# Performance work log

Hardware: AMD Instinct MI355X
Metric: run time of the kernel (lower is better)

## Reference

```python
import jax, jax.numpy as jnp
import numpy as np

A, B, S, E, H = 8, 64, 128, 512, 512


def _xavier(key, shape):
    fan_in, fan_out = shape[-2], shape[-1]
    limit = float(np.sqrt(6.0 / (fan_in + fan_out)))
    return jax.random.uniform(key, shape, jnp.float32, -limit, limit)


def setup_inputs() -> dict:
    key = jax.random.key(0)
    ks = jax.random.split(key, 8)
    inp = {
        "x": jax.random.normal(ks[0], (A, B, S, E), jnp.float32),
        "input2r": _xavier(ks[1], (A, E, H)),
        "input2z": _xavier(ks[2], (A, E, H)),
        "input2n": _xavier(ks[3], (A, E, H)),
        "hidden2r": _xavier(ks[4], (A, H, H)),
        "hidden2z": _xavier(ks[5], (A, H, H)),
        "hidden2n": _xavier(ks[6], (A, H, H)),
        "input2r_bias": jnp.zeros((A, H), jnp.float32),
        "input2z_bias": jnp.zeros((A, H), jnp.float32),
        "input2n_bias": jnp.zeros((A, H), jnp.float32),
        "hidden2r_bias": jnp.zeros((A, H), jnp.float32),
        "hidden2z_bias": jnp.zeros((A, H), jnp.float32),
        "hidden2n_bias": jnp.zeros((A, H), jnp.float32),
    }
    return inp


def _gru(x, input2r, input2z, input2n, input2r_bias, input2z_bias, input2n_bias,
         hidden2r, hidden2z, hidden2n, hidden2r_bias, hidden2z_bias, hidden2n_bias):
    # Precompute the input projections for all timesteps at once (same math,
    # hoisted out of the sequential loop): [A,B,S,H] -> scan over S.
    xr = jnp.einsum('abse,aeh->absh', x, input2r) + input2r_bias[:, None, None, :]
    xz = jnp.einsum('abse,aeh->absh', x, input2z) + input2z_bias[:, None, None, :]
    xn = jnp.einsum('abse,aeh->absh', x, input2n) + input2n_bias[:, None, None, :]
    # scan carries h: [A,B,H]; inputs have leading S axis.
    xr_t = jnp.moveaxis(xr, 2, 0)  # [S,A,B,H]
    xz_t = jnp.moveaxis(xz, 2, 0)
    xn_t = jnp.moveaxis(xn, 2, 0)

    hrb = hidden2r_bias[:, None, :]
    hzb = hidden2z_bias[:, None, :]
    hnb = hidden2n_bias[:, None, :]

    def step(h, inputs):
        xr_i, xz_i, xn_i = inputs
        r = jax.nn.sigmoid(xr_i + jnp.einsum('abh,ahk->abk', h, hidden2r) + hrb)
        z = jax.nn.sigmoid(xz_i + jnp.einsum('abh,ahk->abk', h, hidden2z) + hzb)
        n = jnp.tanh(xn_i + r * (jnp.einsum('abh,ahk->abk', h, hidden2n) + hnb))
        h_new = (1.0 - z) * n + z * h
        return h_new, h_new

    h0 = jnp.zeros((x.shape[0], x.shape[1], hidden2r.shape[-1]), x.dtype)
    h_last, outs = jax.lax.scan(step, h0, (xr_t, xz_t, xn_t))
    outputs = jnp.moveaxis(outs, 0, 2)  # [A,B,S,H]
    return outputs, h_last


def reference(x, input2r, input2z, input2n, input2r_bias, input2z_bias, input2n_bias,
              hidden2r, hidden2z, hidden2n, hidden2r_bias, hidden2z_bias, hidden2n_bias):
    return _gru(x, input2r, input2z, input2n, input2r_bias, input2z_bias, input2n_bias,
                hidden2r, hidden2z, hidden2n, hidden2r_bias, hidden2z_bias, hidden2n_bias)
```

## Files before the change

kernel.cpp:

```cpp
#include <hip/hip_runtime.h>

#define A_ 8
#define B_ 64
#define S_ 128
#define E_ 512
#define H_ 512

typedef float f32x4 __attribute__((ext_vector_type(4)));
typedef short s16x8 __attribute__((ext_vector_type(8)));

__device__ __forceinline__ float sigm(float v)   { return 1.f / (1.f + __expf(-v)); }
__device__ __forceinline__ float tanh_f(float v) { return 2.f / (1.f + __expf(-2.f * v)) - 1.f; }

__device__ __forceinline__ unsigned short f2bf(float f) {
  unsigned u = __builtin_bit_cast(unsigned, f);
  u += 0x7fffu + ((u >> 16) & 1u);
  return (unsigned short)(u >> 16);
}
__device__ __forceinline__ float bf2f(unsigned short b) {
  return __builtin_bit_cast(float, ((unsigned)b) << 16);
}

union U2 { unsigned long long u[2]; s16x8 v; };
union PK { uint4 u; unsigned short h[8]; };
union PH { s16x8 v; unsigned short h[8]; };

__global__ __launch_bounds__(256, 2) void gru_proj(
    const float* __restrict__ x,
    const float* __restrict__ wri, const float* __restrict__ wzi, const float* __restrict__ wni,
    const float* __restrict__ bri, const float* __restrict__ bzi, const float* __restrict__ bni,
    const float* __restrict__ brh, const float* __restrict__ bzh,
    unsigned* __restrict__ xprz, float* __restrict__ xn_arr)
{
  const int n0   = blockIdx.x * 64;
  const int b    = blockIdx.y;
  const int a    = blockIdx.z;
  const int tid  = threadIdx.x;
  const int lane = tid & 63;
  const int wid  = tid >> 6;
  const int l15  = lane & 15;
  const int l4   = lane >> 4;

  const float* xp = x + (size_t)(a * B_ + b) * S_ * E_;

  __shared__ short Af[4096];
  __shared__ short Bf[6144];

  f32x4 acc[3][2][4];
#pragma unroll
  for (int g = 0; g < 3; ++g)
#pragma unroll
    for (int m = 0; m < 2; ++m)
#pragma unroll
      for (int c = 0; c < 4; ++c) acc[g][m][c] = (f32x4){0.f, 0.f, 0.f, 0.f};

  const int am = tid >> 1;
  const int ah = tid & 1;

  for (int kt = 0; kt < E_; kt += 32) {
    const float* ap = xp + (size_t)am * E_ + kt + ah * 16;
    float4 a0 = *(const float4*)(ap);
    float4 a1 = *(const float4*)(ap + 4);
    float4 a2 = *(const float4*)(ap + 8);
    float4 a3 = *(const float4*)(ap + 12);
    PH pa0, pa1;
    pa0.h[0]=f2bf(a0.x); pa0.h[1]=f2bf(a0.y); pa0.h[2]=f2bf(a0.z); pa0.h[3]=f2bf(a0.w);
    pa0.h[4]=f2bf(a1.x); pa0.h[5]=f2bf(a1.y); pa0.h[6]=f2bf(a1.z); pa0.h[7]=f2bf(a1.w);
    pa1.h[0]=f2bf(a2.x); pa1.h[1]=f2bf(a2.y); pa1.h[2]=f2bf(a2.z); pa1.h[3]=f2bf(a2.w);
    pa1.h[4]=f2bf(a3.x); pa1.h[5]=f2bf(a3.y); pa1.h[6]=f2bf(a3.z); pa1.h[7]=f2bf(a3.w);
    int au = (am >> 4) * 64 + (ah * 2) * 16 + (am & 15);
    ((s16x8*)Af)[au]      = pa0.v;
    ((s16x8*)Af)[au + 16] = pa1.v;

#pragma unroll
    for (int ii = 0; ii < 3; ++ii) {
      int idx  = tid + ii * 256;
      int gate = idx >> 8;
      int rem  = idx & 255;
      int l    = rem & 63;
      int col  = n0 + ((rem >> 6) << 4) + (l & 15);
      int kb   = kt + (l >> 4) * 8;
      const float* W = gate == 0 ? wri : gate == 1 ? wzi : wni;
      const float* wp2 = W + (size_t)(a * E_ + kb) * H_ + col;
      PH pb;
#pragma unroll
      for (int j = 0; j < 8; ++j) pb.h[j] = f2bf(wp2[(size_t)j * H_]);
      ((s16x8*)Bf)[idx] = pb.v;
    }
    __syncthreads();

    s16x8 av0 = ((s16x8*)Af)[(wid * 2 + 0) * 64 + lane];
    s16x8 av1 = ((s16x8*)Af)[(wid * 2 + 1) * 64 + lane];
#pragma unroll
    for (int g = 0; g < 3; ++g)
#pragma unroll
      for (int cs = 0; cs < 4; ++cs) {
        s16x8 bv = ((s16x8*)Bf)[g * 256 + cs * 64 + lane];
        acc[g][0][cs] = __builtin_amdgcn_mfma_f32_16x16x32_bf16(av0, bv, acc[g][0][cs], 0, 0, 0);
        acc[g][1][cs] = __builtin_amdgcn_mfma_f32_16x16x32_bf16(av1, bv, acc[g][1][cs], 0, 0, 0);
      }
    __syncthreads();
  }

#pragma unroll
  for (int cs = 0; cs < 4; ++cs) {
    int col = n0 + cs * 16 + l15;
    float br = bri[a * H_ + col] + brh[a * H_ + col];
    float bz = bzi[a * H_ + col] + bzh[a * H_ + col];
    float bn = bni[a * H_ + col];
#pragma unroll
    for (int m = 0; m < 2; ++m) {
#pragma unroll
      for (int i = 0; i < 4; ++i) {
        int srow = wid * 32 + m * 16 + l4 * 4 + i;
        size_t base = ((size_t)(a * S_ + srow) * B_ + b) * H_ + col;
        float rv = acc[0][m][cs][i] + br;
        float zv = acc[1][m][cs][i] + bz;
        float nv = acc[2][m][cs][i] + bn;
        xprz[base]   = (unsigned)f2bf(rv) | ((unsigned)f2bf(zv) << 16);
        xn_arr[base] = nv;
      }
    }
  }
}

__global__ __launch_bounds__(256, 1) void gru_scan(
    const unsigned* __restrict__ xprz, const float* __restrict__ xn_arr,
    const float* __restrict__ wrh, const float* __restrict__ wzh, const float* __restrict__ wnh,
    const float* __restrict__ bnh,
    float* __restrict__ out, float* __restrict__ hlast,
    unsigned short* __restrict__ hbuf0, unsigned short* __restrict__ hbuf1,
    int* __restrict__ flags)
{
  __shared__ uint4 wflat[6144];

  const int wg    = blockIdx.x;
  const int G     = wg & 15;
  const int a     = G >> 1;
  const int hf    = G & 1;
  const int slice = wg >> 4;
  const int tid   = threadIdx.x;
  const int lane  = tid & 63;
  const int w     = tid >> 6;
  const int l15   = lane & 15;
  const int l4    = lane >> 4;
  const int mt    = w & 1;
  const int nt    = w >> 1;

  for (int idx = tid; idx < 6144; idx += 256) {
    int gate = idx >> 11;
    int rem  = idx & 2047;
    int kk   = rem >> 7;
    int rem2 = rem & 127;
    int nt_  = rem2 >> 6;
    int l    = rem2 & 63;
    int col   = slice * 32 + nt_ * 16 + (l & 15);
    int kbase = kk * 32 + (l >> 4) * 8;
    const float* W = gate == 0 ? wrh : gate == 1 ? wzh : wnh;
    const float* wp = W + ((size_t)(a * H_ + kbase)) * H_ + col;
    PK pk;
#pragma unroll
    for (int j = 0; j < 8; ++j) pk.h[j] = f2bf(wp[(size_t)j * H_]);
    wflat[idx] = pk.u;
  }
  __syncthreads();

  const int nc    = slice * 32 + nt * 16 + l15;
  const float vbnh = bnh[a * H_ + nc];
  const int halfb = (a * 2 + hf) * 16384;
  const int hbase = halfb + l4 * 256 + (mt * 16 + l15) * 8;
  int* flagsG = flags + G * (16 * 32);

  float hold[4] = {0.f, 0.f, 0.f, 0.f};
  float xr_[4], xz_[4], xn_[4];

#pragma unroll
  for (int i = 0; i < 4; ++i) {
    int b = hf * 32 + mt * 16 + l4 * 4 + i;
    size_t xo = ((size_t)(a * S_ + 0) * B_ + b) * H_ + nc;
    unsigned prz = xprz[xo];
    xr_[i] = bf2f((unsigned short)(prz & 0xffff));
    xz_[i] = bf2f((unsigned short)(prz >> 16));
    xn_[i] = xn_arr[xo];
  }

  const f32x4 zero4 = {0.f, 0.f, 0.f, 0.f};

  for (int s = 0; s < S_; ++s) {
    const unsigned short* hprev = (s & 1) ? hbuf0 : hbuf1;
    unsigned short*       hcur  = (s & 1) ? hbuf1 : hbuf0;

    U2 hh[16];
#pragma unroll
    for (int kk = 0; kk < 16; ++kk) {
      unsigned long long* p = (unsigned long long*)(hprev + hbase + kk * 1024);
      hh[kk].u[0] = __hip_atomic_load(p,     __ATOMIC_RELAXED, __HIP_MEMORY_SCOPE_AGENT);
      hh[kk].u[1] = __hip_atomic_load(p + 1, __ATOMIC_RELAXED, __HIP_MEMORY_SCOPE_AGENT);
    }
    f32x4 aR = zero4, aZ = zero4, aHN = zero4;
#pragma unroll
    for (int kk = 0; kk < 16; ++kk) {
      s16x8 bR = __builtin_bit_cast(s16x8, wflat[kk * 128        + nt * 64 + lane]);
      s16x8 bZ = __builtin_bit_cast(s16x8, wflat[2048 + kk * 128 + nt * 64 + lane]);
      s16x8 bN = __builtin_bit_cast(s16x8, wflat[4096 + kk * 128 + nt * 64 + lane]);
      aR  = __builtin_amdgcn_mfma_f32_16x16x32_bf16(hh[kk].v, bR, aR, 0, 0, 0);
      aZ  = __builtin_amdgcn_mfma_f32_16x16x32_bf16(hh[kk].v, bZ, aZ, 0, 0, 0);
      aHN = __builtin_amdgcn_mfma_f32_16x16x32_bf16(hh[kk].v, bN, aHN, 0, 0, 0);
    }

    float hn4[4];
#pragma unroll
    for (int i = 0; i < 4; ++i) {
      float rg = sigm(xr_[i] + aR[i]);
      float zg = sigm(xz_[i] + aZ[i]);
      float ng = tanh_f(xn_[i] + rg * (aHN[i] + vbnh));
      hn4[i] = (1.f - zg) * ng + zg * hold[i];
      hold[i] = hn4[i];
    }

#pragma unroll
    for (int i = 0; i < 4; ++i) {
      int r = mt * 16 + l4 * 4 + i;
      unsigned short nb = f2bf(hn4[i]);
      unsigned other = __shfl_xor((unsigned)nb, 1);
      if ((lane & 1) == 0) {
        unsigned val = (unsigned)nb | (other << 16);
        __hip_atomic_store((unsigned*)(hcur + halfb + (nc >> 3) * 256 + r * 8 + (nc & 6)),
                           val, __ATOMIC_RELAXED, __HIP_MEMORY_SCOPE_AGENT);
      }
    }
    __syncthreads();
    asm volatile("" ::: "memory");
    if (tid == 0)
      __hip_atomic_store(flagsG + slice * 32, s + 1,
                         __ATOMIC_RELAXED, __HIP_MEMORY_SCOPE_AGENT);

#pragma unroll
    for (int i = 0; i < 4; ++i) {
      int b = hf * 32 + mt * 16 + l4 * 4 + i;
      out[((size_t)(a * B_ + b) * S_ + s) * H_ + nc] = hn4[i];
    }
    if (s == S_ - 1) {
#pragma unroll
      for (int i = 0; i < 4; ++i) {
        int b = hf * 32 + mt * 16 + l4 * 4 + i;
        hlast[(size_t)(a * B_ + b) * H_ + nc] = hn4[i];
      }
    } else {
#pragma unroll
      for (int i = 0; i < 4; ++i) {
        int b = hf * 32 + mt * 16 + l4 * 4 + i;
        size_t xo = ((size_t)(a * S_ + (s + 1)) * B_ + b) * H_ + nc;
        unsigned prz = xprz[xo];
        xr_[i] = bf2f((unsigned short)(prz & 0xffff));
        xz_[i] = bf2f((unsigned short)(prz >> 16));
        xn_[i] = xn_arr[xo];
      }
      const int target = s + 1;
      for (;;) {
        int v = __hip_atomic_load(flagsG + (lane & 15) * 32,
                                  __ATOMIC_RELAXED, __HIP_MEMORY_SCOPE_AGENT);
        if (__all(v >= target)) break;
      }
      asm volatile("" ::: "memory");
    }
  }
}

__global__ __launch_bounds__(256, 1) void gru_persist(
    const float* __restrict__ x,
    const float* __restrict__ wri, const float* __restrict__ wzi, const float* __restrict__ wni,
    const float* __restrict__ wrh, const float* __restrict__ wzh, const float* __restrict__ wnh,
    const float* __restrict__ bri, const float* __restrict__ bzi, const float* __restrict__ bni,
    const float* __restrict__ brh, const float* __restrict__ bzh, const float* __restrict__ bnh,
    float* __restrict__ out, float* __restrict__ hlast,
    unsigned short* __restrict__ hbuf0, unsigned short* __restrict__ hbuf1,
    int* __restrict__ flags)
{
  __shared__ uint4 wflat[6144];
  const int wg = blockIdx.x, a = wg >> 5, slice = wg & 31, n0 = slice << 4;
  const int tid = threadIdx.x, lane = tid & 63, wid = tid >> 6;
  const int l15 = lane & 15, l4 = lane >> 4, b0w = wid << 4;

  for (int idx = tid; idx < 6144; idx += 256) {
    int set = idx / 3072, rem = idx - set * 3072, gate = rem >> 10;
    int rem2 = rem & 1023, kk = rem2 >> 6, l = rem2 & 63;
    int c = l & 15, kbase = kk * 32 + (l >> 4) * 8;
    const float* W = (set == 0) ? (gate == 0 ? wri : gate == 1 ? wzi : wni)
                                : (gate == 0 ? wrh : gate == 1 ? wzh : wnh);
    const float* wp = W + ((size_t)(a * 512 + kbase)) * 512 + n0 + c;
    PK pk;
#pragma unroll
    for (int j = 0; j < 8; ++j) pk.h[j] = f2bf(wp[(size_t)j * 512]);
    wflat[idx] = pk.u;
  }
  __syncthreads();

  const int nc = n0 + l15;
  const float vbri = bri[a*512+nc], vbzi = bzi[a*512+nc], vbni = bni[a*512+nc];
  const float vbrh = brh[a*512+nc], vbzh = bzh[a*512+nc], vbnh = bnh[a*512+nc];
  const float* xrow = x + (size_t)(a * 64 + b0w + l15) * 65536 + l4 * 8;
  const int hbase = ((a * 64 + l4) * 64 + b0w + l15) * 8;
  int* flagsA = flags + a * 64;
  const f32x4 zero4 = {0.f, 0.f, 0.f, 0.f};
  f32x4 aR, aZ, aXN, aHN;

  auto xpart = [&](int sv) {
    const float* xp = xrow + (size_t)sv * 512;
    aR = zero4; aZ = zero4; aXN = zero4;
#pragma unroll
    for (int kk = 0; kk < 16; ++kk) {
      float4 x0 = *reinterpret_cast<const float4*>(xp + kk * 32);
      float4 x1 = *reinterpret_cast<const float4*>(xp + kk * 32 + 4);
      PH af;
      af.h[0]=f2bf(x0.x); af.h[1]=f2bf(x0.y); af.h[2]=f2bf(x0.z); af.h[3]=f2bf(x0.w);
      af.h[4]=f2bf(x1.x); af.h[5]=f2bf(x1.y); af.h[6]=f2bf(x1.z); af.h[7]=f2bf(x1.w);
      s16x8 bR = __builtin_bit_cast(s16x8, wflat[(kk)*64+lane]);
      s16x8 bZ = __builtin_bit_cast(s16x8, wflat[(16+kk)*64+lane]);
      s16x8 bN = __builtin_bit_cast(s16x8, wflat[(32+kk)*64+lane]);
      aR  = __builtin_amdgcn_mfma_f32_16x16x32_bf16(af.v, bR, aR, 0,0,0);
      aZ  = __builtin_amdgcn_mfma_f32_16x16x32_bf16(af.v, bZ, aZ, 0,0,0);
      aXN = __builtin_amdgcn_mfma_f32_16x16x32_bf16(af.v, bN, aXN, 0,0,0);
    }
  };

  xpart(0);
  for (int s = 0; s < S_; ++s) {
    const unsigned short* hprev = (s & 1) ? hbuf0 : hbuf1;
    unsigned short*       hcur  = (s & 1) ? hbuf1 : hbuf0;
    aHN = zero4;
#pragma unroll
    for (int kk = 0; kk < 16; ++kk) {
      unsigned long long* p = (unsigned long long*)(hprev + hbase + kk * 2048);
      U2 uu;
      uu.u[0] = __hip_atomic_load(p,   __ATOMIC_RELAXED, __HIP_MEMORY_SCOPE_AGENT);
      uu.u[1] = __hip_atomic_load(p+1, __ATOMIC_RELAXED, __HIP_MEMORY_SCOPE_AGENT);
      s16x8 bR = __builtin_bit_cast(s16x8, wflat[(48+kk)*64+lane]);
      s16x8 bZ = __builtin_bit_cast(s16x8, wflat[(64+kk)*64+lane]);
      s16x8 bN = __builtin_bit_cast(s16x8, wflat[(80+kk)*64+lane]);
      aR  = __builtin_amdgcn_mfma_f32_16x16x32_bf16(uu.v, bR, aR, 0,0,0);
      aZ  = __builtin_amdgcn_mfma_f32_16x16x32_bf16(uu.v, bZ, aZ, 0,0,0);
      aHN = __builtin_amdgcn_mfma_f32_16x16x32_bf16(uu.v, bN, aHN, 0,0,0);
    }
#pragma unroll
    for (int i = 0; i < 4; ++i) {
      int r = b0w + l4 * 4 + i;
      unsigned* hop = (unsigned*)(hprev + ((a*64 + (nc>>3))*64 + r)*8 + (nc&6));
      unsigned pair = __hip_atomic_load(hop, __ATOMIC_RELAXED, __HIP_MEMORY_SCOPE_AGENT);
      float hold = bf2f((nc & 1) ? (unsigned short)(pair >> 16) : (unsigned short)(pair & 0xffff));
      float rg = sigm(aR[i] + vbri + vbrh);
      float zg = sigm(aZ[i] + vbzi + vbzh);
      float ng = tanh_f(aXN[i] + vbni + rg * (aHN[i] + vbnh));
      float hnew = (1.f - zg) * ng + zg * hold;
      out[((size_t)(a*64 + r)*128 + s)*512 + nc] = hnew;
      if (s == S_ - 1) hlast[(size_t)(a*64 + r)*512 + nc] = hnew;
      unsigned short nb = f2bf(hnew);
      unsigned other = __shfl_xor((unsigned)nb, 1);
      if ((lane & 1) == 0) {
        unsigned val = (unsigned)nb | (other << 16);
        __hip_atomic_store((unsigned*)(hcur + ((a*64 + (nc>>3))*64 + r)*8 + (nc&6)),
                           val, __ATOMIC_RELAXED, __HIP_MEMORY_SCOPE_AGENT);
      }
    }
    __syncthreads();
    if (tid == 0)
      __hip_atomic_store(flagsA + slice, s + 1, __ATOMIC_RELEASE, __HIP_MEMORY_SCOPE_AGENT);
    if (s < S_ - 1) {
      xpart(s + 1);
      const int target = s + 1;
      for (;;) {
        int v = __hip_atomic_load(flagsA + (lane & 31), __ATOMIC_ACQUIRE, __HIP_MEMORY_SCOPE_AGENT);
        if (__all(v >= target)) break;
        __builtin_amdgcn_s_sleep(1);
      }
    }
  }
}

extern "C" void kernel_launch(void* const* d_in, const int* in_sizes, int n_in,
                              void* d_out, int out_size, void* d_ws, size_t ws_size,
                              hipStream_t stream)
{
  const float* x   = (const float*)d_in[0];
  const float* wri = (const float*)d_in[1];
  const float* wzi = (const float*)d_in[2];
  const float* wni = (const float*)d_in[3];
  const float* wrh = (const float*)d_in[4];
  const float* wzh = (const float*)d_in[5];
  const float* wnh = (const float*)d_in[6];
  const float* bri = (const float*)d_in[7];
  const float* bzi = (const float*)d_in[8];
  const float* bni = (const float*)d_in[9];
  const float* brh = (const float*)d_in[10];
  const float* bzh = (const float*)d_in[11];
  const float* bnh = (const float*)d_in[12];

  float* out   = (float*)d_out;
  float* hlast = out + (size_t)A_ * B_ * S_ * H_;

  const size_t XPRZ  = (size_t)A_ * S_ * B_ * H_;
  const size_t HBUF  = (size_t)A_ * 64 * 64 * 8;
  const size_t FLAGS_B = (size_t)16 * 16 * 32 * sizeof(int);
  const size_t need_new = XPRZ * 4 * 2 + HBUF * 2 * 2 + FLAGS_B;
  const size_t need_old = HBUF * 2 * 2 + 2048;

  if (ws_size >= need_new) {
    unsigned* xprz = (unsigned*)d_ws;
    float* xn_arr  = (float*)((char*)d_ws + XPRZ * 4);
    unsigned short* hbuf0 = (unsigned short*)((char*)d_ws + XPRZ * 8);
    unsigned short* hbuf1 = hbuf0 + HBUF;
    int* flags = (int*)(hbuf1 + HBUF);
    hipMemsetAsync(hbuf0, 0, HBUF * 2 * 2 + FLAGS_B, stream);
    gru_proj<<<dim3(8, 64, 8), 256, 0, stream>>>(x, wri, wzi, wni,
                                                 bri, bzi, bni, brh, bzh,
                                                 xprz, xn_arr);
    gru_scan<<<256, 256, 0, stream>>>(xprz, xn_arr, wrh, wzh, wnh, bnh,
                                      out, hlast, hbuf0, hbuf1, flags);
  } else if (ws_size >= need_old) {
    unsigned short* hbuf0 = (unsigned short*)d_ws;
    unsigned short* hbuf1 = hbuf0 + HBUF;
    int* flags = (int*)(hbuf1 + HBUF);
    hipMemsetAsync(d_ws, 0, need_old, stream);
    gru_persist<<<256, 256, 0, stream>>>(x, wri, wzi, wni, wrh, wzh, wnh,
                                         bri, bzi, bni, brh, bzh, bnh,
                                         out, hlast, hbuf0, hbuf1, flags);
  }
}
```

Before: 764.5 us.

## Pre-convert input weights to bf16 fragments and split scan flag wait into halves

Adds a small kernel that converts the input-projection weights to bf16 once, already laid out as MFMA fragments. The projection kernel then loads these with one vector read per fragment instead of strided fp32 loads and per-block conversion, which were repeated across all 64 batch blocks. In the scan kernel, the hidden state for the next step is now loaded right after the flag wait. The wait is split in two: the first 8 producer flags are checked and their half of h is loaded before waiting on the rest, so loads overlap the remaining synchronisation. This costs an extra launch and workspace for the fragment buffer.

```diff
diff --git a/kernel.cpp b/kernel.cpp
--- a/kernel.cpp
+++ b/kernel.cpp
@@ -25,14 +25,41 @@
 union PK { uint4 u; unsigned short h[8]; };
 union PH { s16x8 v; unsigned short h[8]; };
 
+__global__ __launch_bounds__(256) void gru_wconv(
+    const float* __restrict__ wri, const float* __restrict__ wzi,
+    const float* __restrict__ wni, s16x8* __restrict__ wfrag)
+{
+  const int bid = blockIdx.x;
+  const int kt  = bid & 15;
+  const int ag  = bid >> 4;
+  const int g   = ag % 3;
+  const int a   = ag / 3;
+  const float* W = g == 0 ? wri : g == 1 ? wzi : wni;
+  const int t  = threadIdx.x;
+  const int l  = t & 63;
+  const int cs = (t >> 6) & 3;
+  const int colbase = cs * 16 + (l & 15);
+  const int kb = kt * 32 + (l >> 4) * 8;
+  const float* wp0 = W + (size_t)(a * E_ + kb) * H_;
+#pragma unroll
+  for (int nt = 0; nt < 8; ++nt) {
+    const float* wp = wp0 + nt * 64 + colbase;
+    PH pb;
+#pragma unroll
+    for (int j = 0; j < 8; ++j) pb.h[j] = f2bf(wp[(size_t)j * H_]);
+    wfrag[((size_t)bid * 8 + nt) * 256 + t] = pb.v;
+  }
+}
+
 __global__ __launch_bounds__(256, 2) void gru_proj(
     const float* __restrict__ x,
-    const float* __restrict__ wri, const float* __restrict__ wzi, const float* __restrict__ wni,
+    const s16x8* __restrict__ wfrag,
     const float* __restrict__ bri, const float* __restrict__ bzi, const float* __restrict__ bni,
     const float* __restrict__ brh, const float* __restrict__ bzh,
     unsigned* __restrict__ xprz, float* __restrict__ xn_arr)
 {
-  const int n0   = blockIdx.x * 64;
+  const int ntI  = blockIdx.x;
+  const int n0   = ntI * 64;
   const int b    = blockIdx.y;
   const int a    = blockIdx.z;
   const int tid  = threadIdx.x;
@@ -42,6 +69,7 @@
   const int l4   = lane >> 4;
 
   const float* xp = x + (size_t)(a * B_ + b) * S_ * E_;
+  const s16x8* wfA = wfrag + ((size_t)a * 3) * 16 * 8 * 256;
 
   __shared__ short Af[4096];
   __shared__ short Bf[6144];
@@ -58,6 +86,7 @@
   const int ah = tid & 1;
 
   for (int kt = 0; kt < E_; kt += 32) {
+    const int kti = kt >> 5;
     const float* ap = xp + (size_t)am * E_ + kt + ah * 16;
     float4 a0 = *(const float4*)(ap);
     float4 a1 = *(const float4*)(ap + 4);
@@ -74,18 +103,10 @@
 
 #pragma unroll
     for (int ii = 0; ii < 3; ++ii) {
-      int idx  = tid + ii * 256;
-      int gate = idx >> 8;
-      int rem  = idx & 255;
-      int l    = rem & 63;
-      int col  = n0 + ((rem >> 6) << 4) + (l & 15);
-      int kb   = kt + (l >> 4) * 8;
-      const float* W = gate == 0 ? wri : gate == 1 ? wzi : wni;
-      const float* wp2 = W + (size_t)(a * E_ + kb) * H_ + col;
-      PH pb;
-#pragma unroll
-      for (int j = 0; j < 8; ++j) pb.h[j] = f2bf(wp2[(size_t)j * H_]);
-      ((s16x8*)Bf)[idx] = pb.v;
+      int idx = tid + ii * 256;
+      int g   = idx >> 8;
+      int rem = idx & 255;
+      ((s16x8*)Bf)[idx] = wfA[(((size_t)g * 16 + kti) * 8 + ntI) * 256 + rem];
     }
     __syncthreads();
 
@@ -186,17 +207,13 @@
 
   const f32x4 zero4 = {0.f, 0.f, 0.f, 0.f};
 
+  U2 hh[16];
+#pragma unroll
+  for (int kk = 0; kk < 16; ++kk) { hh[kk].u[0] = 0ull; hh[kk].u[1] = 0ull; }
+
   for (int s = 0; s < S_; ++s) {
-    const unsigned short* hprev = (s & 1) ? hbuf0 : hbuf1;
-    unsigned short*       hcur  = (s & 1) ? hbuf1 : hbuf0;
-
-    U2 hh[16];
-#pragma unroll
-    for (int kk = 0; kk < 16; ++kk) {
-      unsigned long long* p = (unsigned long long*)(hprev + hbase + kk * 1024);
-      hh[kk].u[0] = __hip_atomic_load(p,     __ATOMIC_RELAXED, __HIP_MEMORY_SCOPE_AGENT);
-      hh[kk].u[1] = __hip_atomic_load(p + 1, __ATOMIC_RELAXED, __HIP_MEMORY_SCOPE_AGENT);
-    }
+    unsigned short* hcur = (s & 1) ? hbuf1 : hbuf0;
+
     f32x4 aR = zero4, aZ = zero4, aHN = zero4;
 #pragma unroll
     for (int kk = 0; kk < 16; ++kk) {
@@ -258,11 +275,31 @@
       }
       const int target = s + 1;
       for (;;) {
-        int v = __hip_atomic_load(flagsG + (lane & 15) * 32,
+        int v = __hip_atomic_load(flagsG + (lane & 7) * 32,
                                   __ATOMIC_RELAXED, __HIP_MEMORY_SCOPE_AGENT);
         if (__all(v >= target)) break;
       }
       asm volatile("" ::: "memory");
+#pragma unroll
+      for (int kk = 0; kk < 8; ++kk) {
+        const unsigned long long* p =
+            (const unsigned long long*)(hcur + hbase + kk * 1024);
+        hh[kk].u[0] = __hip_atomic_load(p,     __ATOMIC_RELAXED, __HIP_MEMORY_SCOPE_AGENT);
+        hh[kk].u[1] = __hip_atomic_load(p + 1, __ATOMIC_RELAXED, __HIP_MEMORY_SCOPE_AGENT);
+      }
+      for (;;) {
+        int v = __hip_atomic_load(flagsG + ((lane & 7) + 8) * 32,
+                                  __ATOMIC_RELAXED, __HIP_MEMORY_SCOPE_AGENT);
+        if (__all(v >= target)) break;
+      }
+      asm volatile("" ::: "memory");
+#pragma unroll
+      for (int kk = 8; kk < 16; ++kk) {
+        const unsigned long long* p =
+            (const unsigned long long*)(hcur + hbase + kk * 1024);
+        hh[kk].u[0] = __hip_atomic_load(p,     __ATOMIC_RELAXED, __HIP_MEMORY_SCOPE_AGENT);
+        hh[kk].u[1] = __hip_atomic_load(p + 1, __ATOMIC_RELAXED, __HIP_MEMORY_SCOPE_AGENT);
+      }
     }
   }
 }
@@ -398,20 +435,23 @@
   float* out   = (float*)d_out;
   float* hlast = out + (size_t)A_ * B_ * S_ * H_;
 
-  const size_t XPRZ  = (size_t)A_ * S_ * B_ * H_;
-  const size_t HBUF  = (size_t)A_ * 64 * 64 * 8;
+  const size_t XPRZ    = (size_t)A_ * S_ * B_ * H_;
+  const size_t WFRAG   = (size_t)384 * 8 * 256;
+  const size_t HBUF    = (size_t)A_ * 64 * 64 * 8;
   const size_t FLAGS_B = (size_t)16 * 16 * 32 * sizeof(int);
-  const size_t need_new = XPRZ * 4 * 2 + HBUF * 2 * 2 + FLAGS_B;
-  const size_t need_old = HBUF * 2 * 2 + 2048;
+  const size_t need_new = XPRZ * 8 + WFRAG * 16 + HBUF * 4 + FLAGS_B;
+  const size_t need_old = HBUF * 4 + 2048;
 
   if (ws_size >= need_new) {
     unsigned* xprz = (unsigned*)d_ws;
     float* xn_arr  = (float*)((char*)d_ws + XPRZ * 4);
-    unsigned short* hbuf0 = (unsigned short*)((char*)d_ws + XPRZ * 8);
+    s16x8* wfrag   = (s16x8*)((char*)d_ws + XPRZ * 8);
+    unsigned short* hbuf0 = (unsigned short*)((char*)d_ws + XPRZ * 8 + WFRAG * 16);
     unsigned short* hbuf1 = hbuf0 + HBUF;
     int* flags = (int*)(hbuf1 + HBUF);
-    hipMemsetAsync(hbuf0, 0, HBUF * 2 * 2 + FLAGS_B, stream);
-    gru_proj<<<dim3(8, 64, 8), 256, 0, stream>>>(x, wri, wzi, wni,
+    hipMemsetAsync(hbuf0, 0, HBUF * 4 + FLAGS_B, stream);
+    gru_wconv<<<384, 256, 0, stream>>>(wri, wzi, wni, wfrag);
+    gru_proj<<<dim3(8, 64, 8), 256, 0, stream>>>(x, wfrag,
                                                  bri, bzi, bni, brh, bzh,
                                                  xprz, xn_arr);
     gru_scan<<<256, 256, 0, stream>>>(xprz, xn_arr, wrh, wzh, wnh, bnh,
```

Measured after the change: 900.8 us. +17.8%, slower.
